# Kernel optimization log

Measured on AMD Instinct MI355X. Metric: run time of the kernel, lower is better.

## Reference

```python
import jax, jax.numpy as jnp
import numpy as np

F, K, V, ITERS = 150000, 5, 100000, 5
S = 2 ** K  # factor state space
MLP_SIZE = 2 * ITERS * S + ITERS * 2  # 330
NEG = -1e30
SHIFT = -500.0

# static bit table: bits[state, slot] in {0,1}
_BITS = ((np.arange(S)[:, None] >> np.arange(K)[None, :]) & 1).astype(np.int32)  # [S,K]
_BITS_T = jnp.asarray(_BITS.T)  # [K,S]
# mask bias for grouped logsumexp: bias[slot, b, state] = 0 if bits[state,slot]==b else NEG
_BIAS = jnp.asarray(np.where(_BITS.T[:, None, :] == np.arange(2)[None, :, None], 0.0, NEG).astype(np.float32))  # [K,2,S]


def neg_inf_to_zero(x):
    return jnp.where(jnp.isneginf(x), 0.0, x)


def expand(msg):
    # msg [F,K,2] -> [F,K,S]: broadcast each slot message over factor states by that slot's bit
    return msg[:, jnp.arange(K)[:, None], _BITS_T]


def setup_inputs() -> dict:
    key = jax.random.key(0)
    k0, k1 = jax.random.split(key)
    factor_potentials = jax.random.normal(k0, (F, S), dtype=jnp.float32)
    var_idx = jax.random.randint(k1, (F, K), 0, V, dtype=jnp.int32)
    prv_v2f = jnp.zeros((F, K, 2), jnp.float32)
    prv_f2v = jnp.zeros((F, K, 2), jnp.float32)
    prv_fb = jax.nn.log_softmax(factor_potentials, axis=1)
    # bethe MLP initialized exactly as in the torch module
    lin1_w = jnp.eye(MLP_SIZE, dtype=jnp.float32)
    lin1_b = jnp.zeros((MLP_SIZE,), jnp.float32)
    num_ones = 2 * S + 2
    lin2_w = jnp.zeros((1, MLP_SIZE), jnp.float32).at[0, -num_ones:].set(1.0)
    lin2_b = jnp.zeros((1,), jnp.float32)
    return {"factor_potentials": factor_potentials, "var_idx": var_idx,
            "prv_v2f": prv_v2f, "prv_f2v": prv_f2v, "prv_fb": prv_fb,
            "lin1_w": lin1_w, "lin1_b": lin1_b, "lin2_w": lin2_w, "lin2_b": lin2_b}


def _shifted_relu(x):
    return jnp.maximum(x, SHIFT)


def reference(factor_potentials, var_idx, prv_v2f, prv_f2v, prv_fb, lin1_w, lin1_b, lin2_w, lin2_b):
    var_flat = var_idx.reshape(-1)
    deg = jax.ops.segment_sum(jnp.ones((F * K,), jnp.float32), var_flat, num_segments=V)  # var_degrees
    pooled_states = []
    fb, v2f = prv_fb, prv_v2f
    for _ in range(ITERS):
        # factor->var messages, no double counting: subtract the slot's own incoming message
        scores = fb[:, None, :] - expand(v2f)                    # [F,K,S]
        m = jax.nn.logsumexp(scores[:, :, None, :] + _BIAS[None], axis=-1)  # [F,K,2]
        m = jax.nn.log_softmax(m, axis=-1)
        # var beliefs: gather all incoming factor->var messages
        vb = jax.ops.segment_sum(m.reshape(-1, 2), var_flat, num_segments=V)  # [V,2]
        vb = jax.nn.log_softmax(vb, axis=-1)
        # var->factor messages, no double counting
        v2f = jax.nn.log_softmax(vb[var_idx] - m, axis=-1)        # [F,K,2]
        # factor beliefs
        fb = factor_potentials + expand(v2f).sum(axis=1)          # [F,S]
        fb = fb - jax.nn.logsumexp(fb, axis=1, keepdims=True)
        # pooled Bethe free-energy features for this iteration
        e_fb = jnp.exp(fb)
        energy = jnp.sum(e_fb * neg_inf_to_zero(factor_potentials), axis=0)     # [S]
        fac_ent = -jnp.sum(e_fb * neg_inf_to_zero(fb), axis=0)                  # [S]
        var_term = jnp.sum((deg - 1.0)[:, None] * jnp.exp(vb) * neg_inf_to_zero(vb), axis=0)  # [2]
        pooled_states.append(jnp.concatenate([energy, fac_ent, var_term])[None, :])  # [1, 2S+2]
    x = jnp.concatenate(pooled_states, axis=1)   # [1, MLP_SIZE]
    h = _shifted_relu(x @ lin1_w.T + lin1_b)
    out = _shifted_relu(h @ lin2_w.T + lin2_b)   # [1,1] estimated ln(Z)
    return out
```

## Files before the change

### kernel.cpp

```cpp
#include <hip/hip_runtime.h>

#define F_N   150000
#define K_N   5
#define S_N   32
#define V_N   100000
#define NITER 5
#define MLP_N 330
#define SHIFTV (-500.0f)
#define W_ELL 32

#define FBLK  ((F_N + 255) / 256)
#define GBLK  ((V_N * 8 + 255) / 256)
#define BBLK  (6 * FBLK)

__device__ __forceinline__ float lse2(float a, float b) {
    float mx = fmaxf(a, b);
    return mx + __logf(__expf(a - mx) + __expf(b - mx));
}

__global__ __launch_bounds__(256) void k_build(
    const float* __restrict__ prv_fb,
    const float* __restrict__ prv_v2f,
    const int*   __restrict__ vidx,
    float2*      __restrict__ m_out,
    int*         __restrict__ deg,
    int*         __restrict__ ell)
{
    int g = blockIdx.x / 6, r = blockIdx.x % 6;

    if (r < 5) {
        int e = (g * 5 + r) * 256 + threadIdx.x;
        if (e >= F_N * K_N) return;
        int v = vidx[e];
        int f = e / K_N;
        int k = e - f * K_N;
        int pos = atomicAdd(&deg[v], 1);
        if (pos < W_ELL)
            __builtin_nontemporal_store(k * F_N + f, &ell[v * W_ELL + pos]);
        return;
    }

    int f = g * 256 + threadIdx.x;
    if (f >= F_N) return;

    float fb[S_N];
    const float4* p4 = reinterpret_cast<const float4*>(prv_fb + (size_t)f * S_N);
    #pragma unroll
    for (int i = 0; i < S_N / 4; ++i) {
        float4 v = p4[i];
        fb[i*4+0] = v.x; fb[i*4+1] = v.y; fb[i*4+2] = v.z; fb[i*4+3] = v.w;
    }
    float M = fb[0];
    #pragma unroll
    for (int s = 1; s < S_N; ++s) M = fmaxf(M, fb[s]);
    float T = 0.0f;
    float S0[K_N] = {0.f, 0.f, 0.f, 0.f, 0.f};
    #pragma unroll
    for (int s = 0; s < S_N; ++s) {
        float t = __expf(fb[s] - M);
        T += t;
        #pragma unroll
        for (int k = 0; k < K_N; ++k)
            if (((s >> k) & 1) == 0) S0[k] += t;
    }
    #pragma unroll
    for (int k = 0; k < K_N; ++k) {
        float v0 = prv_v2f[(size_t)f * (K_N*2) + k*2 + 0];
        float v1 = prv_v2f[(size_t)f * (K_N*2) + k*2 + 1];
        float u0 = __logf(S0[k])     - v0;
        float u1 = __logf(T - S0[k]) - v1;
        float l  = lse2(u0, u1);
        m_out[k*F_N + f] = make_float2(u0 - l, u1 - l);
    }
}

__global__ __launch_bounds__(256) void k_gather(
    const float2* __restrict__ m,
    const int*    __restrict__ deg,
    const int*    __restrict__ ell,
    float2*       __restrict__ vb,
    float2*       __restrict__ cpart,
    int iter)
{
    __shared__ float2 wred[4];
    int t = blockIdx.x * 256 + threadIdx.x;
    int v = t >> 3, sub = t & 7;
    int lane = threadIdx.x & 63;

    float a0 = 0.0f, a1 = 0.0f;
    int n = 0;
    if (v < V_N) {
        n = deg[v];
        int nn = n < W_ELL ? n : W_ELL;
        const int* row = ell + (size_t)v * W_ELL;
        for (int i = sub; i < nn; i += 8) {
            float2 mm = m[row[i]];
            a0 += mm.x; a1 += mm.y;
        }
    }
    a0 += __shfl_xor(a0, 1); a1 += __shfl_xor(a1, 1);
    a0 += __shfl_xor(a0, 2); a1 += __shfl_xor(a1, 2);
    a0 += __shfl_xor(a0, 4); a1 += __shfl_xor(a1, 4);

    float c0 = 0.0f, c1 = 0.0f;
    if (v < V_N && sub == 0) {
        vb[v] = make_float2(a0, a1);
        float l = lse2(a0, a1);
        float b0 = a0 - l, b1 = a1 - l;
        float dm1 = (float)n - 1.0f;
        c0 = dm1 * __expf(b0) * b0;
        c1 = dm1 * __expf(b1) * b1;
    }
    #pragma unroll
    for (int mk = 32; mk >= 1; mk >>= 1) {
        c0 += __shfl_xor(c0, mk);
        c1 += __shfl_xor(c1, mk);
    }
    if (lane == 0) wred[threadIdx.x >> 6] = make_float2(c0, c1);
    __syncthreads();
    if (threadIdx.x == 0) {
        float2 s = wred[0];
        s.x += wred[1].x + wred[2].x + wred[3].x;
        s.y += wred[1].y + wred[2].y + wred[3].y;
        cpart[iter * GBLK + blockIdx.x] = s;
    }
}

template <bool LAST>
__global__ __launch_bounds__(256) void k_iter(
    const float*  __restrict__ pot,
    const int*    __restrict__ vidx,
    float2*       __restrict__ m,
    const float2* __restrict__ vb,
    float*        __restrict__ fpart,
    int iter)
{
    const int lane = threadIdx.x & 63;
    __shared__ float red[256];

    int f = blockIdx.x * 256 + threadIdx.x;
    bool valid = f < F_N;
    int fc = valid ? f : (F_N - 1);

    float2 mm[K_N];
    #pragma unroll
    for (int k = 0; k < K_N; ++k) mm[k] = m[k*F_N + fc];
    int vi[K_N];
    #pragma unroll
    for (int k = 0; k < K_N; ++k) vi[k] = vidx[(size_t)fc * K_N + k];

    float v2f[K_N][2];
    #pragma unroll
    for (int k = 0; k < K_N; ++k) {
        float2 b = vb[vi[k]];
        float a0 = b.x - mm[k].x;
        float a1 = b.y - mm[k].y;
        float l = lse2(a0, a1);
        v2f[k][0] = a0 - l;
        v2f[k][1] = a1 - l;
    }

    float fb[S_N];
    const float4* p4 = reinterpret_cast<const float4*>(pot + (size_t)fc * S_N);
    #pragma unroll
    for (int i = 0; i < S_N / 4; ++i) {
        float4 pv = p4[i];
        int s = i * 4;
        fb[s+0] = pv.x + v2f[0][(s+0)&1] + v2f[1][((s+0)>>1)&1] + v2f[2][((s+0)>>2)&1] + v2f[3][((s+0)>>3)&1] + v2f[4][((s+0)>>4)&1];
        fb[s+1] = pv.y + v2f[0][(s+1)&1] + v2f[1][((s+1)>>1)&1] + v2f[2][((s+1)>>2)&1] + v2f[3][((s+1)>>3)&1] + v2f[4][((s+1)>>4)&1];
        fb[s+2] = pv.z + v2f[0][(s+2)&1] + v2f[1][((s+2)>>1)&1] + v2f[2][((s+2)>>2)&1] + v2f[3][((s+2)>>3)&1] + v2f[4][((s+2)>>4)&1];
        fb[s+3] = pv.w + v2f[0][(s+3)&1] + v2f[1][((s+3)>>1)&1] + v2f[2][((s+3)>>2)&1] + v2f[3][((s+3)>>3)&1] + v2f[4][((s+3)>>4)&1];
    }

    float M = fb[0];
    #pragma unroll
    for (int s = 1; s < S_N; ++s) M = fmaxf(M, fb[s]);

    float T = 0.0f;
    float S0[K_N] = {0.f, 0.f, 0.f, 0.f, 0.f};
    #pragma unroll
    for (int s = 0; s < S_N; ++s) {
        float t = __expf(fb[s] - M);
        T += t;
        #pragma unroll
        for (int k = 0; k < K_N; ++k)
            if (((s >> k) & 1) == 0) S0[k] += t;
    }

    if (!LAST) {
        #pragma unroll
        for (int k = 0; k < K_N; ++k) {
            float u0 = __logf(S0[k])     - v2f[k][0];
            float u1 = __logf(T - S0[k]) - v2f[k][1];
            float l  = lse2(u0, u1);
            if (valid) m[k*F_N + f] = make_float2(u0 - l, u1 - l);
        }
    }

    float invT = 1.0f / T;
    float logT = __logf(T);
    float arr[2 * S_N];
    #pragma unroll
    for (int s = 0; s < S_N; ++s) {
        float p   = __expf(fb[s] - M) * invT;
        float fbn = fb[s] - M - logT;
        float w   = v2f[0][s&1] + v2f[1][(s>>1)&1] + v2f[2][(s>>2)&1]
                  + v2f[3][(s>>3)&1] + v2f[4][(s>>4)&1];
        float po  = fb[s] - w;
        arr[s]       = valid ? p * po   : 0.0f;
        arr[S_N + s] = valid ? -p * fbn : 0.0f;
    }

    #pragma unroll
    for (int mk = 32; mk >= 1; mk >>= 1) {
        bool upper = (lane & mk) != 0;
        #pragma unroll
        for (int j = 0; j < mk; ++j) {
            float send = upper ? arr[j] : arr[j + mk];
            float recv = __shfl_xor(send, mk);
            float keep = upper ? arr[j + mk] : arr[j];
            arr[j] = keep + recv;
        }
    }

    red[threadIdx.x] = arr[0];
    __syncthreads();
    if (threadIdx.x < 64) {
        float s = red[threadIdx.x] + red[64 + threadIdx.x]
                + red[128 + threadIdx.x] + red[192 + threadIdx.x];
        fpart[((size_t)iter * FBLK + blockIdx.x) * 64 + threadIdx.x] = s;
    }
}

__global__ __launch_bounds__(256) void k_vt(
    const float*  __restrict__ fpart,
    const float2* __restrict__ cpart,
    float*        __restrict__ x)
{
    __shared__ float red[256];
    int b = blockIdx.x, t = threadIdx.x;
    float acc = 0.0f;
    if (b < 320) {
        int it = b >> 6, s = b & 63;
        for (int i = t; i < FBLK; i += 256)
            acc += fpart[((size_t)it * FBLK + i) * 64 + s];
    } else {
        int idx = b - 320;
        int it = idx >> 1, c = idx & 1;
        for (int i = t; i < GBLK; i += 256) {
            float2 p = cpart[it * GBLK + i];
            acc += c ? p.y : p.x;
        }
    }
    red[t] = acc;
    __syncthreads();
    #pragma unroll
    for (int off = 128; off >= 1; off >>= 1) {
        if (t < off) red[t] += red[t + off];
        __syncthreads();
    }
    if (t == 0) {
        if (b < 320) {
            int it = b >> 6, s = b & 63;
            x[it*66 + s] = red[0];
        } else {
            int idx = b - 320;
            int it = idx >> 1, c = idx & 1;
            x[it*66 + 64 + c] = red[0];
        }
    }
}

__global__ __launch_bounds__(64) void k_mlp1(
    const float* __restrict__ x, const float* __restrict__ w1,
    const float* __restrict__ b1, float* __restrict__ h)
{
    int j = blockIdx.x;
    int lane = threadIdx.x;
    float s = 0.0f;
    for (int i = lane; i < MLP_N; i += 64) s += x[i] * w1[(size_t)j * MLP_N + i];
    #pragma unroll
    for (int mk = 32; mk >= 1; mk >>= 1) s += __shfl_xor(s, mk);
    if (lane == 0) h[j] = fmaxf(s + b1[j], SHIFTV);
}

__global__ __launch_bounds__(64) void k_mlp2(
    const float* __restrict__ h, const float* __restrict__ w2,
    const float* __restrict__ b2, float* __restrict__ out)
{
    int lane = threadIdx.x;
    float s = 0.0f;
    for (int i = lane; i < MLP_N; i += 64) s += h[i] * w2[i];
    #pragma unroll
    for (int mk = 32; mk >= 1; mk >>= 1) s += __shfl_xor(s, mk);
    if (lane == 0) out[0] = fmaxf(s + b2[0], SHIFTV);
}

extern "C" void kernel_launch(void* const* d_in, const int* in_sizes, int n_in,
                              void* d_out, int out_size, void* d_ws, size_t ws_size,
                              hipStream_t stream)
{
    (void)in_sizes; (void)n_in; (void)out_size; (void)ws_size;
    const float* pot  = (const float*)d_in[0];
    const int*   vidx = (const int*)  d_in[1];
    const float* pv2f = (const float*)d_in[2];
    const float* pfb  = (const float*)d_in[4];
    const float* w1   = (const float*)d_in[5];
    const float* b1   = (const float*)d_in[6];
    const float* w2   = (const float*)d_in[7];
    const float* b2   = (const float*)d_in[8];

    float2* m     = (float2*)d_ws;
    float2* vb    = m + 5 * F_N;
    float2* cpart = vb + V_N;
    float*  fpart = (float*)(cpart + NITER * GBLK);
    float*  x     = fpart + (size_t)NITER * FBLK * 64;
    float*  h     = x + MLP_N;
    int*    ell   = (int*)(h + MLP_N);
    int*    deg   = ell + (size_t)V_N * W_ELL;

    hipMemsetAsync(deg, 0, V_N * sizeof(int), stream);

    k_build<<<BBLK, 256, 0, stream>>>(pfb, pv2f, vidx, m, deg, ell);

    for (int it = 0; it < NITER; ++it) {
        k_gather<<<GBLK, 256, 0, stream>>>(m, deg, ell, vb, cpart, it);
        if (it < NITER - 1)
            k_iter<false><<<FBLK, 256, 0, stream>>>(pot, vidx, m, vb, fpart, it);
        else
            k_iter<true><<<FBLK, 256, 0, stream>>>(pot, vidx, m, vb, fpart, it);
    }

    k_vt<<<330, 256, 0, stream>>>(fpart, cpart, x);
    k_mlp1<<<MLP_N, 64, 0, stream>>>(x, w1, b1, h);
    k_mlp2<<<1, 64, 0, stream>>>(h, w2, b2, (float*)d_out);
}
```

Baseline: 203.3 us.

## Scatter messages into per-variable ELL slots so gather reads contiguously

Instead of storing edge indices in an ELL table and doing an indirect load of each message during the per-variable gather, the build pass records each edge's ELL slot position. The factor kernel then writes each new message both to its factor-major array and directly into the variable's ELL row, so the gather reads contiguous float2 rows. The degree counters are padded to reduce atomic contention on shared cache lines. This trades the gather's random reads for random scattered writes in the factor kernel, plus an extra scatter kernel and a larger degree memset.

After: 206.0 us. No clear change (+1.3%).

```diff
diff --git a/kernel.cpp b/kernel.cpp
--- a/kernel.cpp
+++ b/kernel.cpp
@@ -8,9 +8,11 @@
 #define MLP_N 330
 #define SHIFTV (-500.0f)
 #define W_ELL 32
+#define DEG_PAD 16
 
 #define FBLK  ((F_N + 255) / 256)
 #define GBLK  ((V_N * 8 + 255) / 256)
+#define EBLK  ((F_N * K_N + 255) / 256)
 #define BBLK  (6 * FBLK)
 
 __device__ __forceinline__ float lse2(float a, float b) {
@@ -24,7 +26,7 @@
     const int*   __restrict__ vidx,
     float2*      __restrict__ m_out,
     int*         __restrict__ deg,
-    int*         __restrict__ ell)
+    int*         __restrict__ ellpos)
 {
     int g = blockIdx.x / 6, r = blockIdx.x % 6;
 
@@ -32,11 +34,8 @@
         int e = (g * 5 + r) * 256 + threadIdx.x;
         if (e >= F_N * K_N) return;
         int v = vidx[e];
-        int f = e / K_N;
-        int k = e - f * K_N;
-        int pos = atomicAdd(&deg[v], 1);
-        if (pos < W_ELL)
-            __builtin_nontemporal_store(k * F_N + f, &ell[v * W_ELL + pos]);
+        int pos = atomicAdd(&deg[v * DEG_PAD], 1);
+        ellpos[e] = (pos < W_ELL) ? v * W_ELL + pos : V_N * W_ELL;
         return;
     }
 
@@ -74,10 +73,21 @@
     }
 }
 
+__global__ __launch_bounds__(256) void k_scatter0(
+    const int*    __restrict__ ellpos,
+    const float2* __restrict__ m,
+    float2*       __restrict__ mell)
+{
+    int e = blockIdx.x * 256 + threadIdx.x;
+    if (e >= F_N * K_N) return;
+    int f = e / K_N;
+    int k = e - f * K_N;
+    mell[ellpos[e]] = m[k * F_N + f];
+}
+
 __global__ __launch_bounds__(256) void k_gather(
-    const float2* __restrict__ m,
+    const float2* __restrict__ mell,
     const int*    __restrict__ deg,
-    const int*    __restrict__ ell,
     float2*       __restrict__ vb,
     float2*       __restrict__ cpart,
     int iter)
@@ -90,11 +100,11 @@
     float a0 = 0.0f, a1 = 0.0f;
     int n = 0;
     if (v < V_N) {
-        n = deg[v];
+        n = deg[v * DEG_PAD];
         int nn = n < W_ELL ? n : W_ELL;
-        const int* row = ell + (size_t)v * W_ELL;
+        const float2* row = mell + (size_t)v * W_ELL;
         for (int i = sub; i < nn; i += 8) {
-            float2 mm = m[row[i]];
+            float2 mm = row[i];
             a0 += mm.x; a1 += mm.y;
         }
     }
@@ -130,7 +140,9 @@
 __global__ __launch_bounds__(256) void k_iter(
     const float*  __restrict__ pot,
     const int*    __restrict__ vidx,
+    const int*    __restrict__ ellpos,
     float2*       __restrict__ m,
+    float2*       __restrict__ mell,
     const float2* __restrict__ vb,
     float*        __restrict__ fpart,
     int iter)
@@ -188,12 +200,19 @@
     }
 
     if (!LAST) {
+        int el[K_N];
+        #pragma unroll
+        for (int k = 0; k < K_N; ++k) el[k] = ellpos[(size_t)fc * K_N + k];
         #pragma unroll
         for (int k = 0; k < K_N; ++k) {
             float u0 = __logf(S0[k])     - v2f[k][0];
             float u1 = __logf(T - S0[k]) - v2f[k][1];
             float l  = lse2(u0, u1);
-            if (valid) m[k*F_N + f] = make_float2(u0 - l, u1 - l);
+            if (valid) {
+                float2 nm = make_float2(u0 - l, u1 - l);
+                m[k*F_N + f] = nm;
+                mell[el[k]]  = nm;
+            }
         }
     }
 
@@ -310,25 +329,27 @@
     const float* w2   = (const float*)d_in[7];
     const float* b2   = (const float*)d_in[8];
 
-    float2* m     = (float2*)d_ws;
-    float2* vb    = m + 5 * F_N;
-    float2* cpart = vb + V_N;
-    float*  fpart = (float*)(cpart + NITER * GBLK);
-    float*  x     = fpart + (size_t)NITER * FBLK * 64;
-    float*  h     = x + MLP_N;
-    int*    ell   = (int*)(h + MLP_N);
-    int*    deg   = ell + (size_t)V_N * W_ELL;
-
-    hipMemsetAsync(deg, 0, V_N * sizeof(int), stream);
-
-    k_build<<<BBLK, 256, 0, stream>>>(pfb, pv2f, vidx, m, deg, ell);
+    float2* m      = (float2*)d_ws;
+    float2* mell   = m + 5 * F_N;
+    float2* vb     = mell + (size_t)V_N * W_ELL + 32;
+    float2* cpart  = vb + V_N;
+    float*  fpart  = (float*)(cpart + NITER * GBLK);
+    float*  x      = fpart + (size_t)NITER * FBLK * 64;
+    float*  h      = x + MLP_N;
+    int*    ellpos = (int*)(h + MLP_N);
+    int*    deg    = ellpos + (size_t)F_N * K_N;
+
+    hipMemsetAsync(deg, 0, (size_t)V_N * DEG_PAD * sizeof(int), stream);
+
+    k_build<<<BBLK, 256, 0, stream>>>(pfb, pv2f, vidx, m, deg, ellpos);
+    k_scatter0<<<EBLK, 256, 0, stream>>>(ellpos, m, mell);
 
     for (int it = 0; it < NITER; ++it) {
-        k_gather<<<GBLK, 256, 0, stream>>>(m, deg, ell, vb, cpart, it);
+        k_gather<<<GBLK, 256, 0, stream>>>(mell, deg, vb, cpart, it);
         if (it < NITER - 1)
-            k_iter<false><<<FBLK, 256, 0, stream>>>(pot, vidx, m, vb, fpart, it);
+            k_iter<false><<<FBLK, 256, 0, stream>>>(pot, vidx, ellpos, m, mell, vb, fpart, it);
         else
-            k_iter<true><<<FBLK, 256, 0, stream>>>(pot, vidx, m, vb, fpart, it);
+            k_iter<true><<<FBLK, 256, 0, stream>>>(pot, vidx, ellpos, m, mell, vb, fpart, it);
     }
 
     k_vt<<<330, 256, 0, stream>>>(fpart, cpart, x);
```
